# Performance work log

Measured on AMD Instinct MI355X. Metric: run time of the kernel, lower is better.

Reference implementation:

```python
import jax, jax.numpy as jnp
import numpy as np

B, T, C = 4, 2048, 768
H, KVH, D = 6, 6, 128
HALF = D // 2


def setup_inputs() -> dict:
    key = jax.random.key(0)
    ks = jax.random.split(key, 5)
    x = jax.random.normal(ks[0], (B, T, C), dtype=jnp.float32)
    # true rotary frequencies
    inv_freq = 1.0 / (10000.0 ** (jnp.arange(HALF, dtype=jnp.float32) / HALF))
    ang = jnp.arange(T, dtype=jnp.float32)[:, None] * inv_freq[None, :]  # [T, HALF]
    cos, sin = jnp.cos(ang), jnp.sin(ang)
    s = 0.02
    wq = jax.random.normal(ks[1], (H * D, C), dtype=jnp.float32) * s
    wk = jax.random.normal(ks[2], (KVH * D, C), dtype=jnp.float32) * s
    wv = jax.random.normal(ks[3], (KVH * D, C), dtype=jnp.float32) * s
    wproj = jax.random.normal(ks[4], (C, C), dtype=jnp.float32) * s
    return {"x": x, "cos": cos, "sin": sin, "wq": wq, "wk": wk, "wv": wv, "wproj": wproj}


def _norm(t, eps=1e-6):
    # torch: (x - mean) / (std + eps), std unbiased (ddof=1)
    mean = jnp.mean(t, axis=-1, keepdims=True)
    var = jnp.sum((t - mean) ** 2, axis=-1, keepdims=True) / (t.shape[-1] - 1)
    return (t - mean) / (jnp.sqrt(var) + eps)


def _rope(t, cos, sin):
    # t: [B, T, heads, D]; cos/sin: [T, HALF]
    x1, x2 = t[..., :HALF], t[..., HALF:]
    c = cos[None, :, None, :]
    s = sin[None, :, None, :]
    return jnp.concatenate([x1 * c + x2 * s, -x1 * s + x2 * c], axis=-1)


def reference(x, cos, sin, wq, wk, wv, wproj):
    q = jnp.einsum('btc,oc->bto', x, wq).reshape(B, T, H, D)
    k = jnp.einsum('btc,oc->bto', x, wk).reshape(B, T, KVH, D)
    v = jnp.einsum('btc,oc->bto', x, wv).reshape(B, T, KVH, D)
    q = _norm(_rope(q, cos, sin))
    k = _norm(_rope(k, cos, sin))
    # -> [B, heads, T, D]
    q = q.transpose(0, 2, 1, 3)
    k = k.transpose(0, 2, 1, 3)
    v = v.transpose(0, 2, 1, 3)
    # nrep = H // KVH == 1, repeat_kv is a no-op here
    scale = 1.0 / jnp.sqrt(jnp.float32(D))
    scores = jnp.einsum('bhtd,bhsd->bhts', q, k) * scale  # [B,H,T,T]
    causal = jnp.tril(jnp.ones((T, T), dtype=bool))
    scores = jnp.where(causal[None, None], scores, jnp.float32(-1e30))
    attn = jax.nn.softmax(scores, axis=-1)
    y = jnp.einsum('bhts,bhsd->bhtd', attn, v)
    y = y.transpose(0, 2, 1, 3).reshape(B, T, H * D)
    return jnp.einsum('bto,co->btc', y, wproj)
```

## Files before the change

kernel.cpp:

```cpp
#include <hip/hip_runtime.h>

#define BB 4
#define TT 2048
#define CC 768
#define HH 6
#define DD 128
#define BT (BB * TT)
#define HALF 64
#define NBH (BB * HH)
#define QKSCALE 0.12753785627919282f

typedef __bf16 v8bf __attribute__((ext_vector_type(8)));
typedef float f32x4 __attribute__((ext_vector_type(4)));

__device__ __forceinline__ unsigned short f2b(float f) {
  union { float f; unsigned u; } v; v.f = f;
  unsigned r = v.u + 0x7FFFu + ((v.u >> 16) & 1u);
  return (unsigned short)(r >> 16);
}
__device__ __forceinline__ float b2f(unsigned short u) {
  union { unsigned u; float f; } v; v.u = (unsigned)u << 16;
  return v.f;
}
__device__ __forceinline__ unsigned pk2(float f0, float f1) {
  union { float f; unsigned u; } a, b; a.f = f1; b.f = f0;
  return __builtin_amdgcn_perm(a.u, b.u, 0x07060302u);
}
__device__ __forceinline__ float ex2(float x) {
  float r; asm("v_exp_f32 %0, %1" : "=v"(r) : "v"(x)); return r;
}

__device__ __forceinline__ void load_lds16(const void* g, void* l) {
  __builtin_amdgcn_global_load_lds(
      (const __attribute__((address_space(1))) unsigned int*)g,
      (__attribute__((address_space(3))) unsigned int*)(unsigned int)(unsigned long long)(l),
      16, 0, 0);
}

__global__ __launch_bounds__(256) void cvt_all_kernel(const float* __restrict__ x,
                                                      const float* __restrict__ w0,
                                                      const float* __restrict__ w1,
                                                      const float* __restrict__ w2,
                                                      const float* __restrict__ w3,
                                                      unsigned short* __restrict__ xb,
                                                      unsigned short* __restrict__ wb) {
  int bx = blockIdx.x;
  const float* src;
  unsigned short* dst;
  int i;
  if (bx < 6144) {
    src = x; dst = xb; i = bx * 256 + threadIdx.x;
  } else {
    int bsel = (bx - 6144) / 576;
    src = bsel == 0 ? w0 : bsel == 1 ? w1 : bsel == 2 ? w2 : w3;
    dst = wb + bsel * 589824;
    i = ((bx - 6144) % 576) * 256 + threadIdx.x;
  }
  float4 f = ((const float4*)src)[i];
  ushort4 o;
  o.x = f2b(f.x); o.y = f2b(f.y); o.z = f2b(f.z); o.w = f2b(f.w);
  ((ushort4*)dst)[i] = o;
}

__global__ __launch_bounds__(256) void gemm_qkv(const unsigned short* __restrict__ A,
                                                const unsigned short* __restrict__ Wall,
                                                unsigned short* __restrict__ qb,
                                                unsigned short* __restrict__ kb,
                                                unsigned short* __restrict__ vt) {
  __shared__ __align__(16) unsigned short As[2][512 * 8];
  __shared__ __align__(16) unsigned short Bs[2][512 * 8];
  const int m0 = blockIdx.x * 128;
  const int wsel = blockIdx.y / HH, h = blockIdx.y % HH;
  const unsigned short* W = Wall + (size_t)wsel * 589824 + (size_t)h * 128 * CC;
  const int tid = threadIdx.x;
  const int wave = tid >> 6, lane = tid & 63;
  const int fr = lane & 15, quad = lane >> 4;
  const int wm = (wave & 1) * 64, wn = (wave >> 1) * 64;

  f32x4 acc[4][4];
#pragma unroll
  for (int i = 0; i < 4; i++)
#pragma unroll
    for (int j = 0; j < 4; j++) acc[i][j] = (f32x4){0.f, 0.f, 0.f, 0.f};

  auto stage = [&](int kk, int buf) {
#pragma unroll
    for (int it = 0; it < 2; it++) {
      int base_slot = wave * 128 + it * 64;
      int sigma = base_slot + lane;
      int r = sigma >> 2, g = (sigma & 3) ^ ((r >> 1) & 3);
      load_lds16(A + (size_t)(m0 + r) * CC + kk + g * 8, &As[buf][base_slot * 8]);
      load_lds16(W + (size_t)r * CC + kk + g * 8, &Bs[buf][base_slot * 8]);
    }
  };

  stage(0, 0);
  __syncthreads();
  for (int step = 0; step < CC / 32; step++) {
    int buf = step & 1;
    if (step + 1 < CC / 32) stage((step + 1) * 32, buf ^ 1);
    v8bf af[4], bfr[4];
#pragma unroll
    for (int i = 0; i < 4; i++) {
      int ra = wm + i * 16 + fr;
      af[i] = *(const v8bf*)&As[buf][(4 * ra + (quad ^ ((ra >> 1) & 3))) * 8];
      int rb = wn + i * 16 + fr;
      bfr[i] = *(const v8bf*)&Bs[buf][(4 * rb + (quad ^ ((rb >> 1) & 3))) * 8];
    }
#pragma unroll
    for (int i = 0; i < 4; i++)
#pragma unroll
      for (int j = 0; j < 4; j++)
        acc[i][j] = __builtin_amdgcn_mfma_f32_16x16x32_bf16(af[i], bfr[j], acc[i][j], 0, 0, 0);
    __syncthreads();
  }

  if (wsel < 2) {
    unsigned short* dst = wsel ? kb : qb;
#pragma unroll
    for (int i = 0; i < 4; i++) {
      int rr0 = m0 + wm + i * 16 + quad * 4;
      int b = rr0 >> 11, t0 = rr0 & 2047;
      size_t base = ((size_t)(b * HH + h) * TT + t0) * DD;
#pragma unroll
      for (int j = 0; j < 4; j++) {
        int d = wn + j * 16 + fr;
#pragma unroll
        for (int r = 0; r < 4; r++)
          dst[base + (size_t)r * DD + d] = f2b(acc[i][j][r]);
      }
    }
  } else {
#pragma unroll
    for (int i = 0; i < 4; i++) {
      int rr0 = m0 + wm + i * 16 + quad * 4;
      int b = rr0 >> 11, t0_ = rr0 & 2047;
      int bh = b * HH + h;
      int jt = t0_ >> 5;
      int qv = (t0_ >> 3) & 3;
      int jj = t0_ & 7;
#pragma unroll
      for (int j = 0; j < 4; j++) {
        int d = wn + j * 16 + fr;
        int lane_v = qv * 16 + (d & 15);
        size_t off = ((size_t)(bh * 64 + jt) * 8 + (d >> 4)) * 512 + lane_v * 8 + jj;
        ushort4 u = { f2b(acc[i][j][0]), f2b(acc[i][j][1]),
                      f2b(acc[i][j][2]), f2b(acc[i][j][3]) };
        *(ushort4*)&vt[off] = u;
      }
    }
  }
}

__global__ __launch_bounds__(256) void gemm_w64(const unsigned short* __restrict__ A,
                                                const unsigned short* __restrict__ W,
                                                float* __restrict__ C) {
  __shared__ __align__(16) unsigned short As[2][256 * 8];
  __shared__ __align__(16) unsigned short Bs[2][512 * 8];
  const int m0 = blockIdx.x * 64, n0 = blockIdx.y * 128;
  const int tid = threadIdx.x;
  const int wave = tid >> 6, lane = tid & 63;
  const int fr = lane & 15, quad = lane >> 4;
  const int wm = (wave & 1) * 32, wn = (wave >> 1) * 64;

  f32x4 acc[2][4];
#pragma unroll
  for (int i = 0; i < 2; i++)
#pragma unroll
    for (int j = 0; j < 4; j++) acc[i][j] = (f32x4){0.f, 0.f, 0.f, 0.f};

  auto stage = [&](int kk, int buf) {
    {
      int base_slot = wave * 64;
      int sigma = base_slot + lane;
      int r = sigma >> 2, g = (sigma & 3) ^ ((r >> 1) & 3);
      load_lds16(A + (size_t)(m0 + r) * CC + kk + g * 8, &As[buf][base_slot * 8]);
    }
#pragma unroll
    for (int it = 0; it < 2; it++) {
      int base_slot = wave * 128 + it * 64;
      int sigma = base_slot + lane;
      int r = sigma >> 2, g = (sigma & 3) ^ ((r >> 1) & 3);
      load_lds16(W + (size_t)(n0 + r) * CC + kk + g * 8, &Bs[buf][base_slot * 8]);
    }
  };

  stage(0, 0);
  __syncthreads();
  for (int step = 0; step < CC / 32; step++) {
    int buf = step & 1;
    if (step + 1 < CC / 32) stage((step + 1) * 32, buf ^ 1);
    v8bf af[2], bfr[4];
#pragma unroll
    for (int i = 0; i < 2; i++) {
      int ra = wm + i * 16 + fr;
      af[i] = *(const v8bf*)&As[buf][(4 * ra + (quad ^ ((ra >> 1) & 3))) * 8];
    }
#pragma unroll
    for (int j = 0; j < 4; j++) {
      int rb = wn + j * 16 + fr;
      bfr[j] = *(const v8bf*)&Bs[buf][(4 * rb + (quad ^ ((rb >> 1) & 3))) * 8];
    }
#pragma unroll
    for (int i = 0; i < 2; i++)
#pragma unroll
      for (int j = 0; j < 4; j++)
        acc[i][j] = __builtin_amdgcn_mfma_f32_16x16x32_bf16(af[i], bfr[j], acc[i][j], 0, 0, 0);
    __syncthreads();
  }

  const int orow = m0 + wm + quad * 4;
#pragma unroll
  for (int i = 0; i < 2; i++)
#pragma unroll
    for (int j = 0; j < 4; j++) {
      int oc = n0 + wn + j * 16 + fr;
#pragma unroll
      for (int r = 0; r < 4; r++)
        C[(size_t)(orow + i * 16 + r) * CC + oc] = acc[i][j][r];
    }
}

__global__ __launch_bounds__(256) void rope_all_kernel(unsigned short* __restrict__ qb,
                                                       const unsigned short* __restrict__ kb,
                                                       const float* __restrict__ cosb,
                                                       const float* __restrict__ sinb,
                                                       unsigned short* __restrict__ k2) {
  int bx = blockIdx.x;
  bool isq = (bx < 12288);
  const unsigned short* src = isq ? qb : kb;
  float scale = isq ? QKSCALE : 1.0f;
  int idx = (bx % 12288) * 4 + (threadIdx.x >> 6);
  int lane = threadIdx.x & 63;
  int tpos = idx & (TT - 1);
  size_t base = (size_t)idx * DD;

  float x1 = b2f(src[base + lane]);
  float x2 = b2f(src[base + HALF + lane]);
  float c = cosb[tpos * HALF + lane];
  float s = sinb[tpos * HALF + lane];
  float o1 = x1 * c + x2 * s;
  float o2 = x2 * c - x1 * s;

  float sum = o1 + o2;
#pragma unroll
  for (int off = 32; off; off >>= 1) sum += __shfl_xor(sum, off);
  float mean = sum * (1.f / 128.f);
  float d1 = o1 - mean, d2 = o2 - mean;
  float vs = d1 * d1 + d2 * d2;
#pragma unroll
  for (int off = 32; off; off >>= 1) vs += __shfl_xor(vs, off);
  float inv = scale / (sqrtf(vs * (1.f / 127.f)) + 1e-6f);

  if (isq) {
    qb[base + lane] = f2b(d1 * inv);
    qb[base + HALF + lane] = f2b(d2 * inv);
  } else {
    int bh = idx >> 11, t = idx & 2047;
    int jt = t >> 5, rr = t & 31;
    int half = rr >> 4, frv = rr & 15;
    int q5 = (lane >> 3) & 3, j = lane & 7, kb1 = lane >> 5;
    size_t b2 = (size_t)bh * 262144 + (size_t)jt * 4096 + half * 512 + q5 * 128 + frv * 8 + j;
    k2[b2 + (size_t)kb1 * 1024] = f2b(d1 * inv);
    k2[b2 + (size_t)(kb1 + 2) * 1024] = f2b(d2 * inv);
  }
}

__global__ __launch_bounds__(256) void attn_mfma(const unsigned short* __restrict__ qtb,
                                                 const unsigned short* __restrict__ k2b,
                                                 const unsigned short* __restrict__ v2b,
                                                 unsigned short* __restrict__ Opart,
                                                 float* __restrict__ lpart) {
  const int u = blockIdx.x;
  const int bh = u % NBH;
  const int uu = u / NBH;
  int qt, c;
  if (uu < 16)      { c = 0; qt = 15 - uu; }
  else if (uu < 28) { c = 1; qt = 31 - uu; }
  else if (uu < 36) { c = 2; qt = 43 - uu; }
  else              { c = 3; qt = 51 - uu; }
  const int t0 = c * 16;
  const int t1 = min(t0 + 16, 4 * qt + 4);
  const int niter = t1 - t0;

  const int tid = threadIdx.x;
  const int wave = tid >> 6, lane = tid & 63;
  const int fr = lane & 15, quad = lane >> 4;
  const int idxf = 4 * ((quad & 1) * 32 + fr);
  const int idxs = idxf + 64;
  const size_t head_base = (size_t)bh * TT * DD;
  const int m0 = qt * 128 + wave * 32;

  const unsigned short* k2h = k2b + (size_t)bh * 262144;
  const unsigned short* v2h = v2b + (size_t)bh * 262144;

  v8bf qf[2][4];
#pragma unroll
  for (int qs = 0; qs < 2; qs++)
#pragma unroll
    for (int kbk = 0; kbk < 4; kbk++)
      qf[qs][kbk] = *(const v8bf*)(qtb + head_base +
                                   (size_t)(m0 + qs * 16 + fr) * DD + kbk * 32 + quad * 8);

  const __bf16 one_bf = (__bf16)1.0f;
  v8bf ones = {one_bf, one_bf, one_bf, one_bf, one_bf, one_bf, one_bf, one_bf};

  f32x4 oacc[2][8];
#pragma unroll
  for (int qs = 0; qs < 2; qs++)
#pragma unroll
    for (int i = 0; i < 8; i++) oacc[qs][i] = (f32x4){0.f, 0.f, 0.f, 0.f};
  f32x4 lacc[2] = {(f32x4){0.f, 0.f, 0.f, 0.f}, (f32x4){0.f, 0.f, 0.f, 0.f}};

  for (int it = 0; it < niter; it++) {
    const int jt = t0 + it;
    const int j0 = jt * 32;
    if (j0 > m0 + 31) continue;

    const unsigned short* kp = k2h + (size_t)jt * 4096 + lane * 8;
    v8bf kf[8];
#pragma unroll
    for (int i = 0; i < 8; i++) kf[i] = *(const v8bf*)&kp[i * 512];
    const unsigned short* vp = v2h + (size_t)jt * 4096 + lane * 8;
    v8bf vf[8];
#pragma unroll
    for (int i = 0; i < 8; i++) vf[i] = *(const v8bf*)&vp[i * 512];

    f32x4 st[2][2];
#pragma unroll
    for (int qs = 0; qs < 2; qs++) { st[qs][0] = (f32x4){0,0,0,0}; st[qs][1] = (f32x4){0,0,0,0}; }
    __builtin_amdgcn_s_setprio(1);
#pragma unroll
    for (int kbk = 0; kbk < 4; kbk++) {
      st[0][0] = __builtin_amdgcn_mfma_f32_16x16x32_bf16(kf[kbk * 2],     qf[0][kbk], st[0][0], 0, 0, 0);
      st[0][1] = __builtin_amdgcn_mfma_f32_16x16x32_bf16(kf[kbk * 2 + 1], qf[0][kbk], st[0][1], 0, 0, 0);
      st[1][0] = __builtin_amdgcn_mfma_f32_16x16x32_bf16(kf[kbk * 2],     qf[1][kbk], st[1][0], 0, 0, 0);
      st[1][1] = __builtin_amdgcn_mfma_f32_16x16x32_bf16(kf[kbk * 2 + 1], qf[1][kbk], st[1][1], 0, 0, 0);
    }
    __builtin_amdgcn_s_setprio(0);

    const bool diag = (j0 + 31 > m0);
    v8bf pa0, pa1;
#pragma unroll
    for (int qs = 0; qs < 2; qs++) {
      float p[8];
      if (diag) {
        const int qrow = m0 + qs * 16 + fr;
#pragma unroll
        for (int r = 0; r < 4; r++) {
          int c0 = j0 + quad * 4 + r;
          p[r]     = (c0      <= qrow) ? ex2(st[qs][0][r]) : 0.f;
          p[4 + r] = (c0 + 16 <= qrow) ? ex2(st[qs][1][r]) : 0.f;
        }
      } else {
#pragma unroll
        for (int r = 0; r < 4; r++) { p[r] = ex2(st[qs][0][r]); p[4 + r] = ex2(st[qs][1][r]); }
      }
      unsigned A0 = pk2(p[0], p[1]), A1 = pk2(p[2], p[3]);
      unsigned B0 = pk2(p[4], p[5]), B1 = pk2(p[6], p[7]);
      unsigned alo0 = (unsigned)__builtin_amdgcn_ds_bpermute(idxf, (int)A0);
      unsigned alo1 = (unsigned)__builtin_amdgcn_ds_bpermute(idxf, (int)A1);
      unsigned ahi0 = (unsigned)__builtin_amdgcn_ds_bpermute(idxs, (int)A0);
      unsigned ahi1 = (unsigned)__builtin_amdgcn_ds_bpermute(idxs, (int)A1);
      unsigned blo0 = (unsigned)__builtin_amdgcn_ds_bpermute(idxf, (int)B0);
      unsigned blo1 = (unsigned)__builtin_amdgcn_ds_bpermute(idxf, (int)B1);
      unsigned bhi0 = (unsigned)__builtin_amdgcn_ds_bpermute(idxs, (int)B0);
      unsigned bhi1 = (unsigned)__builtin_amdgcn_ds_bpermute(idxs, (int)B1);
      const bool ql = (quad < 2);
      union { unsigned w[4]; v8bf v; } pw;
      pw.w[0] = ql ? alo0 : blo0;
      pw.w[1] = ql ? alo1 : blo1;
      pw.w[2] = ql ? ahi0 : bhi0;
      pw.w[3] = ql ? ahi1 : bhi1;
      if (qs == 0) pa0 = pw.v; else pa1 = pw.v;
    }

    __builtin_amdgcn_s_setprio(1);
#pragma unroll
    for (int nt2 = 0; nt2 < 8; nt2++) {
      oacc[0][nt2] = __builtin_amdgcn_mfma_f32_16x16x32_bf16(pa0, vf[nt2], oacc[0][nt2], 0, 0, 0);
      oacc[1][nt2] = __builtin_amdgcn_mfma_f32_16x16x32_bf16(pa1, vf[nt2], oacc[1][nt2], 0, 0, 0);
    }
    lacc[0] = __builtin_amdgcn_mfma_f32_16x16x32_bf16(pa0, ones, lacc[0], 0, 0, 0);
    lacc[1] = __builtin_amdgcn_mfma_f32_16x16x32_bf16(pa1, ones, lacc[1], 0, 0, 0);
    __builtin_amdgcn_s_setprio(0);
  }

  unsigned short* Oc = Opart + (size_t)c * (NBH * TT * DD) + head_base;
#pragma unroll
  for (int qs = 0; qs < 2; qs++) {
#pragma unroll
    for (int nt2 = 0; nt2 < 8; nt2++)
#pragma unroll
      for (int r = 0; r < 4; r++)
        Oc[(size_t)(m0 + qs * 16 + quad * 4 + r) * DD + nt2 * 16 + fr] = f2b(oacc[qs][nt2][r]);
    if (fr == 0) {
#pragma unroll
      for (int r = 0; r < 4; r++)
        lpart[c * (NBH * TT) + bh * TT + m0 + qs * 16 + quad * 4 + r] = lacc[qs][r];
    }
  }
}

__global__ __launch_bounds__(256) void combine_kernel(const unsigned short* __restrict__ Opart,
                                                      const float* __restrict__ lpart,
                                                      unsigned short* __restrict__ yb) {
  int idx = blockIdx.x * 256 + threadIdx.x;
  int row = idx >> 5;
  int dg = (idx & 31) * 4;
  int t = row & 2047;
  int qt = t >> 7;
  int nc = (4 * qt + 4 + 15) >> 4;

  float a0 = 0.f, a1 = 0.f, a2 = 0.f, a3 = 0.f, l = 0.f;
  for (int cchunk = 0; cchunk < nc; cchunk++) {
    ushort4 o = *(const ushort4*)&Opart[(size_t)cchunk * (NBH * TT * DD) + (size_t)row * DD + dg];
    a0 += b2f(o.x); a1 += b2f(o.y); a2 += b2f(o.z); a3 += b2f(o.w);
    l += lpart[cchunk * (NBH * TT) + row];
  }
  float linv = 1.f / l;
  int bh = row >> 11;
  int b = bh / HH, h = bh % HH;
  ushort4 uo = { f2b(a0 * linv), f2b(a1 * linv), f2b(a2 * linv), f2b(a3 * linv) };
  *(ushort4*)&yb[((size_t)(b * TT + t)) * CC + h * DD + dg] = uo;
}

extern "C" void kernel_launch(void* const* d_in, const int* in_sizes, int n_in,
                              void* d_out, int out_size, void* d_ws, size_t ws_size,
                              hipStream_t stream) {
  const float* x     = (const float*)d_in[0];
  const float* cosb  = (const float*)d_in[1];
  const float* sinb  = (const float*)d_in[2];
  const float* wq    = (const float*)d_in[3];
  const float* wk    = (const float*)d_in[4];
  const float* wv    = (const float*)d_in[5];
  const float* wproj = (const float*)d_in[6];
  float* out = (float*)d_out;

  char* w = (char*)d_ws;
  unsigned short* q_t   = (unsigned short*)(w);
  unsigned short* k_t   = (unsigned short*)(w + 12582912);
  float*          lpart = (float*)(w + 12582912);
  unsigned short* v_t   = (unsigned short*)(w + 25165824);
  unsigned short* yb    = (unsigned short*)(w + 37748736);
  unsigned short* xb    = (unsigned short*)(w + 50331648);
  unsigned short* K2    = (unsigned short*)(w + 50331648);
  unsigned short* wb    = (unsigned short*)(w + 62914560);
  unsigned short* Opart = (unsigned short*)(w + 67633152);

  cvt_all_kernel<<<8448, 256, 0, stream>>>(x, wq, wk, wv, wproj, xb, wb);

  gemm_qkv<<<dim3(BT / 128, 3 * HH), 256, 0, stream>>>(xb, wb, q_t, k_t, v_t);

  rope_all_kernel<<<24576, 256, 0, stream>>>(q_t, k_t, cosb, sinb, K2);

  attn_mfma<<<960, 256, 0, stream>>>(q_t, K2, v_t, Opart, lpart);
  combine_kernel<<<6144, 256, 0, stream>>>(Opart, lpart, yb);

  gemm_w64<<<dim3(BT / 64, CC / 128), 256, 0, stream>>>(yb, wb + 3 * 589824, out);
}
```

Before: 234.2 us.

## Double-buffer K tiles in registers and trim per-wave causal loop bound

The attention loop becomes software-pipelined. The next K tile is loaded into a second register buffer while the current tile's QK^T, softmax and PV MFMAs run, with the loop unrolled by two to alternate buffers. Each wave also gets its own trip count, so it stops at its causal diagonal instead of iterating and skipping fully masked tiles. The cost is 32 more VGPRs per thread for the extra K buffer, which could lower occupancy or cause spills.

```diff
diff --git a/kernel.cpp b/kernel.cpp
--- a/kernel.cpp
+++ b/kernel.cpp
@@ -281,7 +281,6 @@
   else              { c = 3; qt = 51 - uu; }
   const int t0 = c * 16;
   const int t1 = min(t0 + 16, 4 * qt + 4);
-  const int niter = t1 - t0;
 
   const int tid = threadIdx.x;
   const int wave = tid >> 6, lane = tid & 63;
@@ -291,6 +290,8 @@
   const size_t head_base = (size_t)bh * TT * DD;
   const int m0 = qt * 128 + wave * 32;
 
+  const int nw = min(t1, 4 * qt + wave + 1) - t0;
+
   const unsigned short* k2h = k2b + (size_t)bh * 262144;
   const unsigned short* v2h = v2b + (size_t)bh * 262144;
 
@@ -312,79 +313,93 @@
     for (int i = 0; i < 8; i++) oacc[qs][i] = (f32x4){0.f, 0.f, 0.f, 0.f};
   f32x4 lacc[2] = {(f32x4){0.f, 0.f, 0.f, 0.f}, (f32x4){0.f, 0.f, 0.f, 0.f}};
 
-  for (int it = 0; it < niter; it++) {
-    const int jt = t0 + it;
-    const int j0 = jt * 32;
-    if (j0 > m0 + 31) continue;
-
-    const unsigned short* kp = k2h + (size_t)jt * 4096 + lane * 8;
-    v8bf kf[8];
-#pragma unroll
-    for (int i = 0; i < 8; i++) kf[i] = *(const v8bf*)&kp[i * 512];
-    const unsigned short* vp = v2h + (size_t)jt * 4096 + lane * 8;
-    v8bf vf[8];
-#pragma unroll
-    for (int i = 0; i < 8; i++) vf[i] = *(const v8bf*)&vp[i * 512];
-
-    f32x4 st[2][2];
-#pragma unroll
-    for (int qs = 0; qs < 2; qs++) { st[qs][0] = (f32x4){0,0,0,0}; st[qs][1] = (f32x4){0,0,0,0}; }
-    __builtin_amdgcn_s_setprio(1);
-#pragma unroll
-    for (int kbk = 0; kbk < 4; kbk++) {
-      st[0][0] = __builtin_amdgcn_mfma_f32_16x16x32_bf16(kf[kbk * 2],     qf[0][kbk], st[0][0], 0, 0, 0);
-      st[0][1] = __builtin_amdgcn_mfma_f32_16x16x32_bf16(kf[kbk * 2 + 1], qf[0][kbk], st[0][1], 0, 0, 0);
-      st[1][0] = __builtin_amdgcn_mfma_f32_16x16x32_bf16(kf[kbk * 2],     qf[1][kbk], st[1][0], 0, 0, 0);
-      st[1][1] = __builtin_amdgcn_mfma_f32_16x16x32_bf16(kf[kbk * 2 + 1], qf[1][kbk], st[1][1], 0, 0, 0);
-    }
-    __builtin_amdgcn_s_setprio(0);
-
-    const bool diag = (j0 + 31 > m0);
-    v8bf pa0, pa1;
-#pragma unroll
-    for (int qs = 0; qs < 2; qs++) {
-      float p[8];
-      if (diag) {
-        const int qrow = m0 + qs * 16 + fr;
-#pragma unroll
-        for (int r = 0; r < 4; r++) {
-          int c0 = j0 + quad * 4 + r;
-          p[r]     = (c0      <= qrow) ? ex2(st[qs][0][r]) : 0.f;
-          p[4 + r] = (c0 + 16 <= qrow) ? ex2(st[qs][1][r]) : 0.f;
-        }
-      } else {
-#pragma unroll
-        for (int r = 0; r < 4; r++) { p[r] = ex2(st[qs][0][r]); p[4 + r] = ex2(st[qs][1][r]); }
-      }
-      unsigned A0 = pk2(p[0], p[1]), A1 = pk2(p[2], p[3]);
-      unsigned B0 = pk2(p[4], p[5]), B1 = pk2(p[6], p[7]);
-      unsigned alo0 = (unsigned)__builtin_amdgcn_ds_bpermute(idxf, (int)A0);
-      unsigned alo1 = (unsigned)__builtin_amdgcn_ds_bpermute(idxf, (int)A1);
-      unsigned ahi0 = (unsigned)__builtin_amdgcn_ds_bpermute(idxs, (int)A0);
-      unsigned ahi1 = (unsigned)__builtin_amdgcn_ds_bpermute(idxs, (int)A1);
-      unsigned blo0 = (unsigned)__builtin_amdgcn_ds_bpermute(idxf, (int)B0);
-      unsigned blo1 = (unsigned)__builtin_amdgcn_ds_bpermute(idxf, (int)B1);
-      unsigned bhi0 = (unsigned)__builtin_amdgcn_ds_bpermute(idxs, (int)B0);
-      unsigned bhi1 = (unsigned)__builtin_amdgcn_ds_bpermute(idxs, (int)B1);
-      const bool ql = (quad < 2);
-      union { unsigned w[4]; v8bf v; } pw;
-      pw.w[0] = ql ? alo0 : blo0;
-      pw.w[1] = ql ? alo1 : blo1;
-      pw.w[2] = ql ? ahi0 : bhi0;
-      pw.w[3] = ql ? ahi1 : bhi1;
-      if (qs == 0) pa0 = pw.v; else pa1 = pw.v;
-    }
-
-    __builtin_amdgcn_s_setprio(1);
-#pragma unroll
-    for (int nt2 = 0; nt2 < 8; nt2++) {
-      oacc[0][nt2] = __builtin_amdgcn_mfma_f32_16x16x32_bf16(pa0, vf[nt2], oacc[0][nt2], 0, 0, 0);
-      oacc[1][nt2] = __builtin_amdgcn_mfma_f32_16x16x32_bf16(pa1, vf[nt2], oacc[1][nt2], 0, 0, 0);
-    }
-    lacc[0] = __builtin_amdgcn_mfma_f32_16x16x32_bf16(pa0, ones, lacc[0], 0, 0, 0);
-    lacc[1] = __builtin_amdgcn_mfma_f32_16x16x32_bf16(pa1, ones, lacc[1], 0, 0, 0);
-    __builtin_amdgcn_s_setprio(0);
-  }
+  v8bf kfA[8], kfB[8], vf[8];
+
+  {
+    const unsigned short* kp = k2h + (size_t)t0 * 4096 + lane * 8;
+#pragma unroll
+    for (int i = 0; i < 8; i++) kfA[i] = *(const v8bf*)&kp[i * 512];
+  }
+
+#define ATTN_STEP(KF, KFN, IT)                                                  \
+  do {                                                                          \
+    const int jt = t0 + (IT);                                                   \
+    const int j0 = jt * 32;                                                     \
+    {                                                                           \
+      const unsigned short* vp = v2h + (size_t)jt * 4096 + lane * 8;            \
+      _Pragma("unroll")                                                         \
+      for (int i = 0; i < 8; i++) vf[i] = *(const v8bf*)&vp[i * 512];           \
+    }                                                                           \
+    if ((IT) + 1 < nw) {                                                        \
+      const unsigned short* kp = k2h + (size_t)(jt + 1) * 4096 + lane * 8;      \
+      _Pragma("unroll")                                                         \
+      for (int i = 0; i < 8; i++) KFN[i] = *(const v8bf*)&kp[i * 512];          \
+    }                                                                           \
+    f32x4 st00 = {0,0,0,0}, st01 = {0,0,0,0}, st10 = {0,0,0,0}, st11 = {0,0,0,0}; \
+    __builtin_amdgcn_s_setprio(1);                                              \
+    _Pragma("unroll")                                                           \
+    for (int kbk = 0; kbk < 4; kbk++) {                                         \
+      st00 = __builtin_amdgcn_mfma_f32_16x16x32_bf16(KF[kbk * 2],     qf[0][kbk], st00, 0, 0, 0); \
+      st01 = __builtin_amdgcn_mfma_f32_16x16x32_bf16(KF[kbk * 2 + 1], qf[0][kbk], st01, 0, 0, 0); \
+      st10 = __builtin_amdgcn_mfma_f32_16x16x32_bf16(KF[kbk * 2],     qf[1][kbk], st10, 0, 0, 0); \
+      st11 = __builtin_amdgcn_mfma_f32_16x16x32_bf16(KF[kbk * 2 + 1], qf[1][kbk], st11, 0, 0, 0); \
+    }                                                                           \
+    __builtin_amdgcn_s_setprio(0);                                              \
+    const bool diag = (j0 + 31 > m0);                                           \
+    v8bf pa0, pa1;                                                              \
+    _Pragma("unroll")                                                           \
+    for (int qs = 0; qs < 2; qs++) {                                            \
+      float p[8];                                                               \
+      f32x4 s0 = qs ? st10 : st00, s1 = qs ? st11 : st01;                       \
+      if (diag) {                                                               \
+        const int qrow = m0 + qs * 16 + fr;                                     \
+        _Pragma("unroll")                                                       \
+        for (int r = 0; r < 4; r++) {                                           \
+          int c0 = j0 + quad * 4 + r;                                           \
+          p[r]     = (c0      <= qrow) ? ex2(s0[r]) : 0.f;                      \
+          p[4 + r] = (c0 + 16 <= qrow) ? ex2(s1[r]) : 0.f;                      \
+        }                                                                       \
+      } else {                                                                  \
+        _Pragma("unroll")                                                       \
+        for (int r = 0; r < 4; r++) { p[r] = ex2(s0[r]); p[4 + r] = ex2(s1[r]); } \
+      }                                                                         \
+      unsigned A0 = pk2(p[0], p[1]), A1 = pk2(p[2], p[3]);                      \
+      unsigned B0 = pk2(p[4], p[5]), B1 = pk2(p[6], p[7]);                      \
+      unsigned alo0 = (unsigned)__builtin_amdgcn_ds_bpermute(idxf, (int)A0);    \
+      unsigned alo1 = (unsigned)__builtin_amdgcn_ds_bpermute(idxf, (int)A1);    \
+      unsigned ahi0 = (unsigned)__builtin_amdgcn_ds_bpermute(idxs, (int)A0);    \
+      unsigned ahi1 = (unsigned)__builtin_amdgcn_ds_bpermute(idxs, (int)A1);    \
+      unsigned blo0 = (unsigned)__builtin_amdgcn_ds_bpermute(idxf, (int)B0);    \
+      unsigned blo1 = (unsigned)__builtin_amdgcn_ds_bpermute(idxf, (int)B1);    \
+      unsigned bhi0 = (unsigned)__builtin_amdgcn_ds_bpermute(idxs, (int)B0);    \
+      unsigned bhi1 = (unsigned)__builtin_amdgcn_ds_bpermute(idxs, (int)B1);    \
+      const bool ql = (quad < 2);                                               \
+      union { unsigned w[4]; v8bf v; } pw;                                      \
+      pw.w[0] = ql ? alo0 : blo0;                                               \
+      pw.w[1] = ql ? alo1 : blo1;                                               \
+      pw.w[2] = ql ? ahi0 : bhi0;                                               \
+      pw.w[3] = ql ? ahi1 : bhi1;                                               \
+      if (qs == 0) pa0 = pw.v; else pa1 = pw.v;                                 \
+    }                                                                           \
+    __builtin_amdgcn_s_setprio(1);                                              \
+    _Pragma("unroll")                                                           \
+    for (int nt2 = 0; nt2 < 8; nt2++) {                                         \
+      oacc[0][nt2] = __builtin_amdgcn_mfma_f32_16x16x32_bf16(pa0, vf[nt2], oacc[0][nt2], 0, 0, 0); \
+      oacc[1][nt2] = __builtin_amdgcn_mfma_f32_16x16x32_bf16(pa1, vf[nt2], oacc[1][nt2], 0, 0, 0); \
+    }                                                                           \
+    lacc[0] = __builtin_amdgcn_mfma_f32_16x16x32_bf16(pa0, ones, lacc[0], 0, 0, 0); \
+    lacc[1] = __builtin_amdgcn_mfma_f32_16x16x32_bf16(pa1, ones, lacc[1], 0, 0, 0); \
+    __builtin_amdgcn_s_setprio(0);                                              \
+  } while (0)
+
+  int it = 0;
+  for (;;) {
+    ATTN_STEP(kfA, kfB, it);
+    if (++it >= nw) break;
+    ATTN_STEP(kfB, kfA, it);
+    if (++it >= nw) break;
+  }
+#undef ATTN_STEP
 
   unsigned short* Oc = Opart + (size_t)c * (NBH * TT * DD) + head_base;
 #pragma unroll
```

Measured after the change: 240.4 us. +2.6%, slower.
